# Kernel optimization log

Measured on AMD Instinct MI355X. Metric: run time of the kernel, lower is better.

The kernel has to match this reference:

```python
import jax, jax.numpy as jnp
import numpy as np

NUM_FORMULAS = 1024
INPUT_DIM = 256
BATCH = 2048


def setup_inputs() -> dict:
    key = jax.random.key(0)
    k_x, k_mu, k_sigma = jax.random.split(key, 3)
    inputs = jax.random.normal(k_x, (BATCH, INPUT_DIM), dtype=jnp.float32)
    # keras random_normal initializer default stddev = 0.05
    mu = 0.05 * jax.random.normal(k_mu, (NUM_FORMULAS, INPUT_DIM), dtype=jnp.float32)
    sigma = 0.05 * jax.random.normal(k_sigma, (1, NUM_FORMULAS, INPUT_DIM), dtype=jnp.float32)
    temperature = jnp.float32(2.0)
    return {"inputs": inputs, "mu": mu, "sigma": sigma, "temperature": temperature}


def reference(inputs, mu, sigma, temperature):
    # diff: (batch, num_formulas, dim)
    diff = inputs[:, None, :] - mu[None, :, :]
    # weighted L2 norm over feature dim -> (batch, num_formulas)
    dist = jnp.sqrt(jnp.sum(jnp.square(diff * sigma), axis=-1))
    loc = jnp.exp(-dist)
    # sigmoid-gated temperature, softmax over formulas (last axis)
    return jax.nn.softmax(jax.nn.sigmoid(temperature) * loc, axis=-1)
```

## Files before the change

### kernel.cpp

```cpp
#include <hip/hip_runtime.h>
#include <math.h>

#define NF 1024
#define DIM 256
#define BATCH 2048
#define K 512
#define BM 64
#define BN 64
#define NCHUNK (NF / BN)

#define WS_A_BYTES (BATCH * K * 2)
#define WS_B_OFF   WS_A_BYTES
#define WS_C_OFF   (WS_A_BYTES + NF * K * 2)
#define WS_RP_OFF  (WS_C_OFF + NF * 4)

typedef __attribute__((ext_vector_type(8))) short short8;
typedef __attribute__((ext_vector_type(4))) float f32x4;

__device__ __forceinline__ unsigned short f2bf(float f) {
    unsigned u = __float_as_uint(f);
    u += 0x7fffu + ((u >> 16) & 1u);
    return (unsigned short)(u >> 16);
}

__device__ __forceinline__ void gl_lds16(const ushort* g, ushort* l) {
    __builtin_amdgcn_global_load_lds(
        (const __attribute__((address_space(1))) void*)g,
        (__attribute__((address_space(3))) void*)l, 16, 0, 0);
}

__global__ __launch_bounds__(256) void k_prep(const float* __restrict__ mu,
                                              const float* __restrict__ sigma,
                                              const float* __restrict__ x,
                                              unsigned int* __restrict__ Ab32,
                                              unsigned int* __restrict__ Bb32,
                                              float* __restrict__ c) {
    const int t = threadIdx.x;
    if (blockIdx.x >= NF) {
        const int i = (blockIdx.x - NF) * 256 + t;
        const float v = x[i];
        Ab32[i] = (unsigned)f2bf(v * v) | ((unsigned)f2bf(v) << 16);
        return;
    }
    const int f = blockIdx.x;
    const float m = mu[f * DIM + t];
    const float s = sigma[f * DIM + t];
    const float s2 = s * s;
    Bb32[f * DIM + t] = (unsigned)f2bf(s2) | ((unsigned)f2bf(-2.0f * s2 * m) << 16);

    float cp = s2 * m * m;
    #pragma unroll
    for (int off = 32; off > 0; off >>= 1) cp += __shfl_down(cp, off, 64);
    __shared__ float red[4];
    const int lane = t & 63, wv = t >> 6;
    if (lane == 0) red[wv] = cp;
    __syncthreads();
    if (t == 0) c[f] = red[0] + red[1] + red[2] + red[3];
}

__global__ __launch_bounds__(256, 2) void k_main(const ushort* __restrict__ Ab,
                                                 const ushort* __restrict__ Bb,
                                                 const float* __restrict__ c,
                                                 const float* __restrict__ temp,
                                                 float* __restrict__ out,
                                                 float* __restrict__ rowPartial) {
    const int t = threadIdx.x;
    const int w = t >> 6;
    const int lane = t & 63;
    const int m16 = lane & 15;
    const int q = lane >> 4;
    const int wr = w >> 1, wc = w & 1;

    const int bid = blockIdx.x;
    const int xcd = bid & 7;
    const int j = bid >> 3;
    const int nc = j & 15;
    const int rb = xcd * 4 + (j >> 4);
    const int r0 = rb * BM;
    const int n0 = nc * BN;

    __shared__ __align__(16) ushort Alds[BM * K];
    __shared__ float sums[4][32];

    #pragma unroll
    for (int i = 0; i < 16; ++i) {
        const int s = i * 256 + t;
        const int row = s >> 6;
        const int kcp = s & 63;
        const int kcl = (kcp & 56) | ((kcp & 7) ^ (row & 7));
        gl_lds16(Ab + (r0 + row) * K + kcl * 8, &Alds[s * 8]);
    }

    f32x4 acc[2][2];
    #pragma unroll
    for (int rt = 0; rt < 2; ++rt)
        #pragma unroll
        for (int ct = 0; ct < 2; ++ct) acc[rt][ct] = (f32x4){0.f, 0.f, 0.f, 0.f};

    const ushort* __restrict__ Brow0 = Bb + (n0 + wc * 32 + m16) * K;
    const ushort* __restrict__ Brow1 = Brow0 + 16 * K;

    __syncthreads();

    #pragma unroll
    for (int ks = 0; ks < K; ks += 32) {
        const int kcq = (ks >> 3) + q;
        short8 av[2], bv[2];
        bv[0] = *(const short8*)&Brow0[ks + q * 8];
        bv[1] = *(const short8*)&Brow1[ks + q * 8];
        #pragma unroll
        for (int jj = 0; jj < 2; ++jj) {
            const int ar = wr * 32 + jj * 16 + m16;
            const int slot = (kcq & 56) | ((kcq & 7) ^ (ar & 7));
            av[jj] = *(const short8*)&Alds[ar * K + slot * 8];
        }
        #pragma unroll
        for (int rt = 0; rt < 2; ++rt)
            #pragma unroll
            for (int ct = 0; ct < 2; ++ct)
                acc[rt][ct] = __builtin_amdgcn_mfma_f32_16x16x32_bf16(
                    av[rt], bv[ct], acc[rt][ct], 0, 0, 0);
    }

    const float g = 1.0f / (1.0f + __expf(-temp[0]));
    #pragma unroll
    for (int rt = 0; rt < 2; ++rt) {
        float s[4] = {0.f, 0.f, 0.f, 0.f};
        #pragma unroll
        for (int ct = 0; ct < 2; ++ct) {
            const int fcol = n0 + wc * 32 + ct * 16 + m16;
            const float cn = c[fcol];
            #pragma unroll
            for (int i = 0; i < 4; ++i) {
                const float dist2 = acc[rt][ct][i] + cn;
                const float dist = sqrtf(fmaxf(dist2, 0.0f));
                const float p = __expf(g * __expf(-dist));
                const int row = r0 + wr * 32 + rt * 16 + q * 4 + i;
                out[row * NF + fcol] = p;
                s[i] += p;
            }
        }
        #pragma unroll
        for (int i = 0; i < 4; ++i) {
            #pragma unroll
            for (int mask = 1; mask < 16; mask <<= 1)
                s[i] += __shfl_xor(s[i], mask, 64);
        }
        if (m16 == 0) {
            #pragma unroll
            for (int i = 0; i < 4; ++i) sums[w][rt * 16 + q * 4 + i] = s[i];
        }
    }
    __syncthreads();
    if (t < BM) {
        const int half = t >> 5, lr = t & 31;
        rowPartial[nc * BATCH + r0 + t] =
            sums[half * 2][lr] + sums[half * 2 + 1][lr];
    }
}

__global__ __launch_bounds__(256) void k_norm(float* __restrict__ out,
                                              const float* __restrict__ rowPartial) {
    const int row = blockIdx.x;
    float ssum = 0.0f;
    #pragma unroll
    for (int ch = 0; ch < NCHUNK; ++ch) ssum += rowPartial[ch * BATCH + row];
    const float inv = 1.0f / ssum;
    float4* o4 = (float4*)(out + row * NF);
    float4 v = o4[threadIdx.x];
    v.x *= inv; v.y *= inv; v.z *= inv; v.w *= inv;
    o4[threadIdx.x] = v;
}

extern "C" void kernel_launch(void* const* d_in, const int* in_sizes, int n_in,
                              void* d_out, int out_size, void* d_ws, size_t ws_size,
                              hipStream_t stream) {
    const float* x     = (const float*)d_in[0];
    const float* mu    = (const float*)d_in[1];
    const float* sigma = (const float*)d_in[2];
    const float* temp  = (const float*)d_in[3];
    float* out = (float*)d_out;

    char* ws = (char*)d_ws;
    ushort* Ab        = (ushort*)ws;
    ushort* Bb        = (ushort*)(ws + WS_B_OFF);
    float*  c         = (float*)(ws + WS_C_OFF);
    float*  rowPartial = (float*)(ws + WS_RP_OFF);

    k_prep<<<NF + BATCH * DIM / 256, 256, 0, stream>>>(mu, sigma, x,
                                                       (unsigned int*)Ab,
                                                       (unsigned int*)Bb, c);

    k_main<<<512, 256, 0, stream>>>(Ab, Bb, c, temp, out, rowPartial);

    k_norm<<<BATCH, 256, 0, stream>>>(out, rowPartial);
}
```

Baseline: 84.71 us.

## Fuse prep, GEMM and normalization into one cooperative kernel with grid syncs

Merges the three kernels (bf16 prep, MFMA distance/exp, row normalization) into one cooperative launch separated by grid.sync barriers. Unnormalized softmax numerators stay in registers across the second barrier, so the output is written once already normalized. This drops the separate read-modify-write pass over the 8 MB output and two launch gaps. In exchange it depends on all 512 blocks being co-resident and pays for two grid-wide barriers.

```diff
diff --git a/kernel.cpp b/kernel.cpp
--- a/kernel.cpp
+++ b/kernel.cpp
@@ -1,5 +1,8 @@
 #include <hip/hip_runtime.h>
+#include <hip/hip_cooperative_groups.h>
 #include <math.h>
+
+namespace cg = cooperative_groups;
 
 #define NF 1024
 #define DIM 256
@@ -8,6 +11,7 @@
 #define BM 64
 #define BN 64
 #define NCHUNK (NF / BN)
+#define GRID 512
 
 #define WS_A_BYTES (BATCH * K * 2)
 #define WS_B_OFF   WS_A_BYTES
@@ -29,49 +33,61 @@
         (__attribute__((address_space(3))) void*)l, 16, 0, 0);
 }
 
-__global__ __launch_bounds__(256) void k_prep(const float* __restrict__ mu,
-                                              const float* __restrict__ sigma,
-                                              const float* __restrict__ x,
-                                              unsigned int* __restrict__ Ab32,
-                                              unsigned int* __restrict__ Bb32,
-                                              float* __restrict__ c) {
+__global__ __launch_bounds__(256, 2) void k_fused(const float* __restrict__ x,
+                                                  const float* __restrict__ mu,
+                                                  const float* __restrict__ sigma,
+                                                  const float* __restrict__ temp,
+                                                  float* __restrict__ out,
+                                                  ushort* __restrict__ Ab,
+                                                  ushort* __restrict__ Bb,
+                                                  float* __restrict__ c,
+                                                  float* __restrict__ rowPartial) {
+    cg::grid_group grid = cg::this_grid();
     const int t = threadIdx.x;
-    if (blockIdx.x >= NF) {
-        const int i = (blockIdx.x - NF) * 256 + t;
-        const float v = x[i];
-        Ab32[i] = (unsigned)f2bf(v * v) | ((unsigned)f2bf(v) << 16);
-        return;
-    }
-    const int f = blockIdx.x;
-    const float m = mu[f * DIM + t];
-    const float s = sigma[f * DIM + t];
-    const float s2 = s * s;
-    Bb32[f * DIM + t] = (unsigned)f2bf(s2) | ((unsigned)f2bf(-2.0f * s2 * m) << 16);
-
-    float cp = s2 * m * m;
-    #pragma unroll
-    for (int off = 32; off > 0; off >>= 1) cp += __shfl_down(cp, off, 64);
+    const int bid = blockIdx.x;
+
+    __shared__ __align__(16) ushort Alds[BM * K];
+    __shared__ float sums[4][32];
+    __shared__ float invRow[BM];
     __shared__ float red[4];
-    const int lane = t & 63, wv = t >> 6;
-    if (lane == 0) red[wv] = cp;
-    __syncthreads();
-    if (t == 0) c[f] = red[0] + red[1] + red[2] + red[3];
-}
-
-__global__ __launch_bounds__(256, 2) void k_main(const ushort* __restrict__ Ab,
-                                                 const ushort* __restrict__ Bb,
-                                                 const float* __restrict__ c,
-                                                 const float* __restrict__ temp,
-                                                 float* __restrict__ out,
-                                                 float* __restrict__ rowPartial) {
-    const int t = threadIdx.x;
+
+    unsigned int* Ab32 = (unsigned int*)Ab;
+    unsigned int* Bb32 = (unsigned int*)Bb;
+
+    {
+        const int lane = t & 63, wv = t >> 6;
+        #pragma unroll
+        for (int ff = 0; ff < 2; ++ff) {
+            const int f = bid * 2 + ff;
+            const float m = mu[f * DIM + t];
+            const float s = sigma[f * DIM + t];
+            const float s2 = s * s;
+            Bb32[f * DIM + t] =
+                (unsigned)f2bf(s2) | ((unsigned)f2bf(-2.0f * s2 * m) << 16);
+            float cp = s2 * m * m;
+            #pragma unroll
+            for (int off = 32; off > 0; off >>= 1) cp += __shfl_down(cp, off, 64);
+            if (lane == 0) red[wv] = cp;
+            __syncthreads();
+            if (t == 0) c[f] = red[0] + red[1] + red[2] + red[3];
+            __syncthreads();
+        }
+        #pragma unroll
+        for (int rr = 0; rr < 4; ++rr) {
+            const int i = (bid * 4 + rr) * DIM + t;
+            const float v = x[i];
+            Ab32[i] = (unsigned)f2bf(v * v) | ((unsigned)f2bf(v) << 16);
+        }
+    }
+
+    grid.sync();
+
     const int w = t >> 6;
     const int lane = t & 63;
     const int m16 = lane & 15;
     const int q = lane >> 4;
     const int wr = w >> 1, wc = w & 1;
 
-    const int bid = blockIdx.x;
     const int xcd = bid & 7;
     const int j = bid >> 3;
     const int nc = j & 15;
@@ -79,9 +95,6 @@
     const int r0 = rb * BM;
     const int n0 = nc * BN;
 
-    __shared__ __align__(16) ushort Alds[BM * K];
-    __shared__ float sums[4][32];
-
     #pragma unroll
     for (int i = 0; i < 16; ++i) {
         const int s = i * 256 + t;
@@ -123,20 +136,19 @@
     }
 
     const float g = 1.0f / (1.0f + __expf(-temp[0]));
+    float preg[2][2][4];
     #pragma unroll
     for (int rt = 0; rt < 2; ++rt) {
         float s[4] = {0.f, 0.f, 0.f, 0.f};
         #pragma unroll
         for (int ct = 0; ct < 2; ++ct) {
-            const int fcol = n0 + wc * 32 + ct * 16 + m16;
-            const float cn = c[fcol];
+            const float cn = c[n0 + wc * 32 + ct * 16 + m16];
             #pragma unroll
             for (int i = 0; i < 4; ++i) {
                 const float dist2 = acc[rt][ct][i] + cn;
                 const float dist = sqrtf(fmaxf(dist2, 0.0f));
                 const float p = __expf(g * __expf(-dist));
-                const int row = r0 + wr * 32 + rt * 16 + q * 4 + i;
-                out[row * NF + fcol] = p;
+                preg[rt][ct][i] = p;
                 s[i] += p;
             }
         }
@@ -157,19 +169,27 @@
         rowPartial[nc * BATCH + r0 + t] =
             sums[half * 2][lr] + sums[half * 2 + 1][lr];
     }
-}
-
-__global__ __launch_bounds__(256) void k_norm(float* __restrict__ out,
-                                              const float* __restrict__ rowPartial) {
-    const int row = blockIdx.x;
-    float ssum = 0.0f;
-    #pragma unroll
-    for (int ch = 0; ch < NCHUNK; ++ch) ssum += rowPartial[ch * BATCH + row];
-    const float inv = 1.0f / ssum;
-    float4* o4 = (float4*)(out + row * NF);
-    float4 v = o4[threadIdx.x];
-    v.x *= inv; v.y *= inv; v.z *= inv; v.w *= inv;
-    o4[threadIdx.x] = v;
+
+    grid.sync();
+
+    if (t < BM) {
+        float ss = 0.0f;
+        #pragma unroll
+        for (int ch = 0; ch < NCHUNK; ++ch) ss += rowPartial[ch * BATCH + r0 + t];
+        invRow[t] = 1.0f / ss;
+    }
+    __syncthreads();
+    #pragma unroll
+    for (int rt = 0; rt < 2; ++rt)
+        #pragma unroll
+        for (int ct = 0; ct < 2; ++ct) {
+            const int fcol = n0 + wc * 32 + ct * 16 + m16;
+            #pragma unroll
+            for (int i = 0; i < 4; ++i) {
+                const int lrow = wr * 32 + rt * 16 + q * 4 + i;
+                out[(r0 + lrow) * NF + fcol] = preg[rt][ct][i] * invRow[lrow];
+            }
+        }
 }
 
 extern "C" void kernel_launch(void* const* d_in, const int* in_sizes, int n_in,
@@ -182,16 +202,14 @@
     float* out = (float*)d_out;
 
     char* ws = (char*)d_ws;
-    ushort* Ab        = (ushort*)ws;
-    ushort* Bb        = (ushort*)(ws + WS_B_OFF);
-    float*  c         = (float*)(ws + WS_C_OFF);
+    ushort* Ab         = (ushort*)ws;
+    ushort* Bb         = (ushort*)(ws + WS_B_OFF);
+    float*  c          = (float*)(ws + WS_C_OFF);
     float*  rowPartial = (float*)(ws + WS_RP_OFF);
 
-    k_prep<<<NF + BATCH * DIM / 256, 256, 0, stream>>>(mu, sigma, x,
-                                                       (unsigned int*)Ab,
-                                                       (unsigned int*)Bb, c);
-
-    k_main<<<512, 256, 0, stream>>>(Ab, Bb, c, temp, out, rowPartial);
-
-    k_norm<<<BATCH, 256, 0, stream>>>(out, rowPartial);
-}
+    void* args[] = {(void*)&x, (void*)&mu, (void*)&sigma, (void*)&temp,
+                    (void*)&out, (void*)&Ab, (void*)&Bb, (void*)&c,
+                    (void*)&rowPartial};
+    hipLaunchCooperativeKernel((const void*)k_fused, dim3(GRID), dim3(256),
+                               args, 0, stream);
+}
```

Result: slower. 180.2 us (+112.7%).
